# Optimization experiments

Hardware: AMD Instinct MI355X
Metric: run time of the kernel (lower is better)

Reference implementation:

```python
import jax, jax.numpy as jnp
import numpy as np

B, N, E, S, A, P, T = 512, 65536, 131072, 256, 512, 2, 64


def setup_inputs() -> dict:
    key = jax.random.key(0)
    ks = jax.random.split(key, 40)
    f32 = jnp.float32

    def g(i, shape, s=0.05):
        return jax.random.normal(ks[i], shape, f32) * s

    inp = {
        'nodes': jax.random.normal(ks[0], (N, S), f32),
        'edge_features': jax.random.normal(ks[1], (E, S), f32),
        'edge_source': jax.random.randint(ks[2], (E,), 0, N),
        'edge_dest': jax.random.randint(ks[3], (E,), 0, N),
        'node_owner': jax.random.randint(ks[4], (N,), 0, B),
        'running': jnp.ones((B,), bool),
        'ref_types': jax.random.randint(ks[5], (B,), 0, T),
        # decision aggregator (transform + sigmoid gate)
        'dec_t_W': g(6, (A, S)), 'dec_t_b': g(7, (A,)),
        'dec_g_W': g(8, (A, S)), 'dec_g_b': jnp.ones((A,), f32),
        # init aggregator
        'init_t_W': g(9, (A, S)), 'init_t_b': g(10, (A,)),
        'init_g_W': g(11, (A, S)), 'init_g_b': jnp.ones((A,), f32),
        # node type decision head + embedding
        'ntd_W': g(12, (T + 1, A)), 'ntd_b': g(13, (T + 1,)),
        'nte': g(14, (T, S), 1.0),
        # f_init
        'f1_W': g(15, (S, S)), 'f1_b': g(16, (S,)),
        'f2_W': g(17, (S, A)),
        # propagator params, stacked over P steps (message_size = 2S)
        'mn_W': g(18, (P, 2 * S, S)),
        'mf_W': g(19, (P, 2 * S, S)),
        'ml2_W': g(20, (P, 2 * S, 2 * S)), 'ml2_b': g(21, (P, 2 * S)),
        'gru_Wih': g(22, (P, 3 * S, 2 * S)), 'gru_Whh': g(23, (P, 3 * S, S)),
        'gru_bih': jnp.zeros((P, 3 * S), f32),
        'gru_bhh': jnp.concatenate(
            [jnp.ones((P, S), f32), jnp.zeros((P, 2 * S), f32)], axis=-1),
    }
    return inp


def _aggregate(nodes, fmask, tW, tb, gW, gb):
    # Aggregator.forward: sigmoid gate * linear transform, pooled per graph
    # via dense 0/1 owner-mask matmul (dropout=0 -> identity).
    gates = jax.nn.sigmoid(nodes @ gW.T + gb)
    data = nodes @ tW.T + tb
    return fmask @ (data * gates)  # [B, A]


def reference(nodes, edge_features, edge_source, edge_dest, node_owner,
              running, ref_types,
              dec_t_W, dec_t_b, dec_g_W, dec_g_b,
              init_t_W, init_t_b, init_g_W, init_g_b,
              ntd_W, ntd_b, nte, f1_W, f1_b, f2_W,
              mn_W, mf_W, ml2_W, ml2_b, gru_Wih, gru_Whh, gru_bih, gru_bhh):
    f32 = nodes.dtype
    fmask = (node_owner[None, :] == jnp.arange(B)[:, None]).astype(f32)  # [B,N]
    # Propagator._node_update_mask: owner_masks[running].sum(0) > 0
    upd = (fmask * running[:, None].astype(f32)).sum(0) > 0  # [N]

    for p in range(P):
        ef = edge_features @ mf_W[p].T                 # [E, 2S]
        nf = nodes @ mn_W[p].T                         # [N, 2S]
        msgs = nf[edge_source] + nf[edge_dest] + ef
        msgs = jnp.tanh(msgs) @ ml2_W[p].T + ml2_b[p]  # message_layer_2
        inputs = jnp.zeros((N, 2 * S), f32)
        inputs = inputs.at[edge_dest].add(msgs).at[edge_source].add(msgs)
        # torch GRUCell (gate order r, z, n)
        gi = inputs @ gru_Wih[p].T + gru_bih[p]
        gh = nodes @ gru_Whh[p].T + gru_bhh[p]
        ir, iz, inn = jnp.split(gi, 3, axis=-1)
        hr, hz, hn = jnp.split(gh, 3, axis=-1)
        r = jax.nn.sigmoid(ir + hr)
        z = jax.nn.sigmoid(iz + hz)
        n = jnp.tanh(inn + r * hn)
        new_nodes = (1.0 - z) * n + z * nodes
        nodes = jnp.where(upd[:, None], new_nodes, nodes)

    # node-type decision
    agg = _aggregate(nodes, fmask, dec_t_W, dec_t_b, dec_g_W, dec_g_b)
    logits = agg @ ntd_W.T + ntd_b                      # [B, T+1]

    # training path: remap_pad (no pad chars present) -> ref + 1
    sel = ref_types + 1                                  # in [1, T]
    logp = jax.nn.log_softmax(logits, axis=-1)
    per_ex = -logp[jnp.arange(B), sel]
    loss = jnp.where(running, per_ex, 0.0).mean()

    # new node features for running graphs
    emb = nte[sel - 1]                                   # [B, S]
    init_feats = _aggregate(nodes, fmask, init_t_W, init_t_b,
                            init_g_W, init_g_b)
    new_features = emb @ f1_W.T + f1_b + init_feats @ f2_W.T  # [B, S]
    return logits, new_features, loss
```

## Files before the change

kernel.cpp:

```cpp
#include <hip/hip_runtime.h>
#include <hip/hip_bf16.h>
#include <math.h>

#define BG 512
#define NN 65536
#define EE 131072
#define SD 256
#define AD 512
#define PP 2
#define TD 64

typedef __attribute__((ext_vector_type(8))) short sx8;
typedef __attribute__((ext_vector_type(4))) short sx4;
typedef __attribute__((ext_vector_type(4))) float fx4;

__device__ __forceinline__ float bs2f(short s) {
    union { unsigned u; float f; } x; x.u = ((unsigned)(unsigned short)s) << 16; return x.f;
}
__device__ __forceinline__ short f2bs(float f) {
    union { float f; unsigned u; } x; x.f = f;
    unsigned r = x.u + 0x7fffu + ((x.u >> 16) & 1u);
    return (short)(r >> 16);
}
__device__ __forceinline__ float fast_tanh(float x) {
    float xc = fminf(fmaxf(x, -15.f), 15.f);
    float e = __expf(2.f * xc);
    return __fdividef(e - 1.f, e + 1.f);
}
__device__ __forceinline__ float fast_sigm(float x) {
    float xc = fminf(fmaxf(x, -30.f), 30.f);
    float e = __expf(-xc);
    return __fdividef(1.f, 1.f + e);
}
__device__ __forceinline__ bool run_flag(const void* runv, int idx) {
    const unsigned char* r8 = (const unsigned char*)runv;
    const int* r32 = (const int*)runv;
    return (r8[idx] != 0) || (r32[idx] != 0);
}

__device__ __forceinline__ void gload16(const short* g, short* l) {
    __builtin_amdgcn_global_load_lds(
        (const __attribute__((address_space(1))) void*)g,
        (__attribute__((address_space(3))) void*)l, 16, 0, 0);
}

template<int EPI>
__launch_bounds__(256, 4)
__global__ void gemm_bt(const short* __restrict__ Abp, const short* __restrict__ Abp2,
                        const short* __restrict__ Wp,
                        const float* __restrict__ bias, const float* __restrict__ bias2,
                        short* __restrict__ Cout, short* __restrict__ Fout,
                        short* __restrict__ FoutB,
                        const float* __restrict__ biasB, const float* __restrict__ biasB2,
                        const int* __restrict__ degp,
                        int K, int Ksp, int NC, int NT, int nsplit)
{
    __shared__ __align__(16) short sA[2 * 4096];
    __shared__ __align__(16) short sB[2 * 4096];
    const int t = threadIdx.x;
    const int lane = t & 63;
    const int w = t >> 6;

    const int nwg = gridDim.x;
    const int q = nwg >> 3;
    const int wg = (blockIdx.x & 7) * q + (blockIdx.x >> 3);
    const int mt = wg / NT;
    const int nt = wg - mt * NT;
    const int m0 = mt * 128;
    const int n0 = nt * 128;

    const int wm = (w >> 1) * 64;
    const int wn = (w & 1) * 64;
    const int lr = lane & 15;
    const int lg = lane >> 4;

    fx4 acc[4][4];
#pragma unroll
    for (int i = 0; i < 4; i++)
#pragma unroll
        for (int j = 0; j < 4; j++) { fx4 z = {0.f, 0.f, 0.f, 0.f}; acc[i][j] = z; }

    const int r = t >> 2;
    const int cblk = (t & 3) ^ ((r >> 1) & 3);
    const short* gA  = Abp  + (size_t)(m0 + r) * Ksp + cblk * 8;
    const short* gA2 = Abp2 + (size_t)(m0 + r) * (K - Ksp) + cblk * 8;
    const short* gB  = Wp + (size_t)(n0 + r) * K + cblk * 8;
    const size_t rsA  = (size_t)64 * Ksp;
    const size_t rsA2 = (size_t)64 * (K - Ksp);
    const size_t rsB  = (size_t)64 * K;

    auto STAGE = [&](int b, int kk) {
        const short* a0 = (kk < Ksp) ? (gA + kk) : (gA2 + (kk - Ksp));
        const size_t rs = (kk < Ksp) ? rsA : rsA2;
        gload16(a0,            sA + b * 4096 + w * 512);
        gload16(a0 + rs,       sA + b * 4096 + 2048 + w * 512);
        gload16(gB + kk,       sB + b * 4096 + w * 512);
        gload16(gB + kk + rsB, sB + b * 4096 + 2048 + w * 512);
    };

    STAGE(0, 0);

    float dgv[4];
    if (EPI == 3) {
#pragma unroll
        for (int mi = 0; mi < 4; mi++)
            dgv[mi] = (float)degp[m0 + wm + mi * 16 + lr];
    }

    __syncthreads();
    int buf = 0;
    const int xa = (lr >> 1) & 3;
    for (int kk = 0; kk < K; kk += 32) {
        if (kk + 32 < K) STAGE(buf ^ 1, kk + 32);
        const short* cA = sA + buf * 4096;
        const short* cB = sB + buf * 4096;
        sx8 af[4], bfr[4];
#pragma unroll
        for (int mi = 0; mi < 4; mi++)
            af[mi] = *(const sx8*)(cA + (wm + mi * 16 + lr) * 32 + (lg ^ xa) * 8);
#pragma unroll
        for (int ni = 0; ni < 4; ni++)
            bfr[ni] = *(const sx8*)(cB + (wn + ni * 16 + lr) * 32 + (lg ^ xa) * 8);
#pragma unroll
        for (int mi = 0; mi < 4; mi++)
#pragma unroll
            for (int ni = 0; ni < 4; ni++) {
                if (EPI == 4)
                    acc[mi][ni] = __builtin_amdgcn_mfma_f32_16x16x32_bf16(
                        af[mi], bfr[ni], acc[mi][ni], 0, 0, 0);
                else
                    acc[mi][ni] = __builtin_amdgcn_mfma_f32_16x16x32_bf16(
                        bfr[ni], af[mi], acc[mi][ni], 0, 0, 0);
            }
        __syncthreads();
        buf ^= 1;
    }

    if (EPI == 4) {
        const bool useB = (n0 >= nsplit);
        short* fo = useB ? FoutB : Fout;
        const float* tb = useB ? biasB : bias;
        const float* gb = useB ? biasB2 : bias2;
        const int ln0 = useB ? (n0 - nsplit) : n0;
#pragma unroll
        for (int mi = 0; mi < 4; mi++) {
#pragma unroll
            for (int rg = 0; rg < 4; rg++) {
                const int m = m0 + wm + mi * 16 + lg * 4 + rg;
#pragma unroll
                for (int ni = 0; ni < 4; ni += 2) {
                    const int rc = (((ln0 + wn + ni * 16) >> 5) << 4) + lr;
                    float dv = acc[mi][ni][rg] + tb[rc];
                    float gv = fast_sigm(acc[mi][ni + 1][rg] + gb[rc]);
                    fo[(size_t)m * 512 + rc] = f2bs(dv * gv);
                }
            }
        }
    } else {
#pragma unroll
        for (int mi = 0; mi < 4; mi++) {
            const int m = m0 + wm + mi * 16 + lr;
            short* co = Cout + (size_t)m * NC + n0;
#pragma unroll
            for (int ni = 0; ni < 4; ni++) {
                const int nc = wn + ni * 16 + lg * 4;
                sx4 o;
                if (EPI == 1) {
#pragma unroll
                    for (int rg = 0; rg < 4; rg++)
                        o[rg] = f2bs(fast_tanh(acc[mi][ni][rg]));
                } else if (EPI == 3) {
                    fx4 bv = *(const fx4*)(bias + n0 + nc);
                    fx4 cv = *(const fx4*)(bias2 + n0 + nc);
#pragma unroll
                    for (int rg = 0; rg < 4; rg++)
                        o[rg] = f2bs(acc[mi][ni][rg] + dgv[mi] * cv[rg] + bv[rg]);
                } else {
                    fx4 vb = {0.f, 0.f, 0.f, 0.f};
                    if (bias) vb = *(const fx4*)(bias + n0 + nc);
#pragma unroll
                    for (int rg = 0; rg < 4; rg++)
                        o[rg] = f2bs(acc[mi][ni][rg] + vb[rg]);
                }
                *(sx4*)(co + nc) = o;
            }
        }
    }
}

__global__ void k_xadd(const short* __restrict__ nodes, const int* __restrict__ esrc,
                       const int* __restrict__ edst, short* __restrict__ X)
{
    size_t idx = ((size_t)blockIdx.x * 256 + threadIdx.x) * 8;
    const int e = (int)(idx >> 8);
    const int j = (int)(idx & 255);
    const int s = esrc[e], d = edst[e];
    sx8 a = *(const sx8*)(nodes + (size_t)s * 256 + j);
    sx8 b = *(const sx8*)(nodes + (size_t)d * 256 + j);
    sx8 o;
#pragma unroll
    for (int u = 0; u < 8; u++) o[u] = f2bs(bs2f(a[u]) + bs2f(b[u]));
    *(sx8*)(X + idx) = o;
}

__global__ void k_castw(const float* __restrict__ in, short* __restrict__ out)
{
    size_t i = ((size_t)blockIdx.x * 256 + threadIdx.x) * 4;
    fx4 v = *(const fx4*)(in + i);
    sx4 o;
#pragma unroll
    for (int u = 0; u < 4; u++) o[u] = f2bs(v[u]);
    *(sx4*)(out + i) = o;
}

__global__ void k_cast_T(const float* __restrict__ in, short* __restrict__ out)
{
    size_t i = ((size_t)blockIdx.x * 256 + threadIdx.x) * 4;
    const int k = (int)(i >> 9);
    const int k2 = (int)(i & 511);
    sx4 o;
#pragma unroll
    for (int u = 0; u < 4; u++) o[u] = f2bs(in[(size_t)(k2 + u) * 512 + k]);
    *(sx4*)(out + i) = o;
}

__global__ void k_vecfuse(const float* __restrict__ Wih, const float* __restrict__ ml2b,
                          float* __restrict__ c1)
{
    const int i = blockIdx.x * 256 + threadIdx.x;
    if (i >= 768) return;
    const float* wr = Wih + (size_t)i * 512;
    float acc = 0.f;
    for (int k = 0; k < 512; k++) acc += wr[k] * ml2b[k];
    c1[i] = acc;
}

__global__ void k_cast_comb(const float* __restrict__ mn, const float* __restrict__ mf,
                            short* __restrict__ out)
{
    size_t i = ((size_t)blockIdx.x * 256 + threadIdx.x) * 4;
    const int n = (int)(i >> 9);
    const int k = (int)(i & 511);
    const float* W = (k < 256) ? (mn + (size_t)n * 256 + k)
                               : (mf + (size_t)n * 256 + (k - 256));
    fx4 v = *(const fx4*)W;
    sx4 o;
#pragma unroll
    for (int u = 0; u < 4; u++) o[u] = f2bs(v[u]);
    *(sx4*)(out + i) = o;
}

__global__ void k_cast_pair(const float* __restrict__ tW, const float* __restrict__ gW,
                            short* __restrict__ out)
{
    size_t i = ((size_t)blockIdx.x * 256 + threadIdx.x) * 4;
    const int r2 = (int)(i >> 8);
    const int c = (int)(i & 255);
    const int src = ((r2 >> 5) << 4) | (r2 & 15);
    const float* W = ((r2 >> 4) & 1) ? gW : tW;
    fx4 v = *(const fx4*)(W + (size_t)src * 256 + c);
    sx4 o;
#pragma unroll
    for (int u = 0; u < 4; u++) o[u] = f2bs(v[u]);
    *(sx4*)(out + i) = o;
}

__global__ void k_count2(const int* __restrict__ a, const int* __restrict__ b,
                         int* __restrict__ deg, int n)
{
    int i = blockIdx.x * 256 + threadIdx.x;
    if (i < n) { atomicAdd(&deg[a[i]], 1); atomicAdd(&deg[b[i]], 1); }
}
__global__ void k_count1(const int* __restrict__ a, int* __restrict__ deg, int n)
{
    int i = blockIdx.x * 256 + threadIdx.x;
    if (i < n) atomicAdd(&deg[a[i]], 1);
}
__global__ void k_scan(const int* __restrict__ deg, int* __restrict__ offs, int n)
{
    __shared__ int part[256];
    const int t = threadIdx.x;
    const int chunk = n >> 8;
    const int base = t * chunk;
    int s = 0;
    for (int i = 0; i < chunk; i++) s += deg[base + i];
    part[t] = s;
    __syncthreads();
    for (int off = 1; off < 256; off <<= 1) {
        int v = (t >= off) ? part[t - off] : 0;
        __syncthreads();
        part[t] += v;
        __syncthreads();
    }
    int run = (t > 0) ? part[t - 1] : 0;
    for (int i = 0; i < chunk; i++) {
        offs[base + i] = run;
        run += deg[base + i];
    }
    if (t == 255) offs[n] = part[255];
}
__global__ void k_fill2(const int* __restrict__ a, const int* __restrict__ b,
                        const int* __restrict__ offs, int* __restrict__ cur,
                        int* __restrict__ elist, int n)
{
    int i = blockIdx.x * 256 + threadIdx.x;
    if (i < n) {
        int p = atomicAdd(&cur[a[i]], 1); elist[offs[a[i]] + p] = i;
        int q = atomicAdd(&cur[b[i]], 1); elist[offs[b[i]] + q] = i;
    }
}
__global__ void k_fill1(const int* __restrict__ own, const int* __restrict__ offs,
                        int* __restrict__ cur, int* __restrict__ nlist, int n)
{
    int i = blockIdx.x * 256 + threadIdx.x;
    if (i < n) {
        int p = atomicAdd(&cur[own[i]], 1); nlist[offs[own[i]] + p] = i;
    }
}

__global__ void k_edge_gather(const short* __restrict__ msgs, const int* __restrict__ offs,
                              const int* __restrict__ elist, short* __restrict__ inp)
{
    const int node = blockIdx.x * 4 + (threadIdx.x >> 6);
    const int c = (threadIdx.x & 63) * 8;
    const int s0 = offs[node], s1 = offs[node + 1];
    float acc[8] = {0.f, 0.f, 0.f, 0.f, 0.f, 0.f, 0.f, 0.f};
    for (int s = s0; s < s1; s++) {
        const int e = elist[s];
        sx8 v = *(const sx8*)(msgs + (size_t)e * 512 + c);
#pragma unroll
        for (int u = 0; u < 8; u++) acc[u] += bs2f(v[u]);
    }
    sx8 o;
#pragma unroll
    for (int u = 0; u < 8; u++) o[u] = f2bs(acc[u]);
    *(sx8*)(inp + (size_t)node * 512 + c) = o;
}

__global__ void k_owner_reduce(const short* __restrict__ gp, const int* __restrict__ offsB,
                               const int* __restrict__ nlist, float* __restrict__ agg)
{
    const int b = blockIdx.x, t = threadIdx.x;
    const int s0 = offsB[b], s1 = offsB[b + 1];
    float a0 = 0.f, a1 = 0.f;
    for (int s = s0; s < s1; s++) {
        const int n = nlist[s];
        const short* pp = gp + (size_t)n * 512 + t * 2;
        a0 += bs2f(pp[0]); a1 += bs2f(pp[1]);
    }
    agg[(size_t)b * 512 + t * 2] = a0;
    agg[(size_t)b * 512 + t * 2 + 1] = a1;
}

__global__ void k_gru(const short* __restrict__ gi, const short* __restrict__ gh,
                      short* __restrict__ nodes,
                      const int* __restrict__ owner, const void* __restrict__ runv)
{
    const int n = blockIdx.x * 4 + (threadIdx.x >> 6);
    const int t = threadIdx.x & 63;
    const bool run = run_flag(runv, owner[n]);
    const size_t gb = (size_t)n * 768 + t * 4;
    sx4 vir = *(const sx4*)(gi + gb);
    sx4 viz = *(const sx4*)(gi + gb + 256);
    sx4 vin = *(const sx4*)(gi + gb + 512);
    sx4 whr = *(const sx4*)(gh + gb);
    sx4 whz = *(const sx4*)(gh + gb + 256);
    sx4 whn = *(const sx4*)(gh + gb + 512);
    const size_t nbase = (size_t)n * 256 + t * 4;
    sx4 old4 = *(const sx4*)(nodes + nbase);
    sx4 outb;
#pragma unroll
    for (int u = 0; u < 4; u++) {
        float old = bs2f(old4[u]);
        float rr = fast_sigm(bs2f(vir[u]) + bs2f(whr[u]));
        float zz = fast_sigm(bs2f(viz[u]) + bs2f(whz[u]));
        float nn = fast_tanh(bs2f(vin[u]) + rr * bs2f(whn[u]));
        float nv = (1.f - zz) * nn + zz * old;
        outb[u] = run ? f2bs(nv) : old4[u];
    }
    *(sx4*)(nodes + nbase) = outb;
}

__global__ void k_logits(const float* __restrict__ agg, const float* __restrict__ Wt,
                         const float* __restrict__ bt, float* __restrict__ logitsF,
                         float* __restrict__ outL)
{
    __shared__ float row[512];
    const int b = blockIdx.x, t = threadIdx.x;
    for (int k = t; k < 512; k += 128) row[k] = agg[(size_t)b * 512 + k];
    __syncthreads();
    if (t < TD + 1) {
        float acc = bt[t];
        const float* wr = Wt + (size_t)t * 512;
        for (int k = 0; k < 512; k++) acc += row[k] * wr[k];
        logitsF[b * (TD + 1) + t] = acc;
        outL[b * (TD + 1) + t] = acc;
    }
}

__global__ void k_loss(const float* __restrict__ logitsF, const int* __restrict__ reft,
                       const void* __restrict__ runv, float* __restrict__ outLoss)
{
    __shared__ float red[512];
    const int b = threadIdx.x;
    const float* lr = logitsF + b * (TD + 1);
    float mx = lr[0];
    for (int k = 1; k < TD + 1; k++) mx = fmaxf(mx, lr[k]);
    float se = 0.f;
    for (int k = 0; k < TD + 1; k++) se += expf(lr[k] - mx);
    const int sel = reft[b] + 1;
    float pe = logf(se) + mx - lr[sel];
    red[b] = run_flag(runv, b) ? pe : 0.f;
    __syncthreads();
    for (int s = 256; s > 0; s >>= 1) {
        if (b < s) red[b] += red[b + s];
        __syncthreads();
    }
    if (b == 0) outLoss[0] = red[0] / (float)BG;
}

__global__ void k_newfeat(const float* __restrict__ aggi, const float* __restrict__ nte,
                          const int* __restrict__ reft, const float* __restrict__ f1W,
                          const float* __restrict__ f1b, const float* __restrict__ f2W,
                          float* __restrict__ outNF)
{
    __shared__ float emb[256];
    __shared__ float ag[512];
    const int b = blockIdx.x, t = threadIdx.x;
    const int rt = reft[b];
    emb[t] = nte[(size_t)rt * 256 + t];
    ag[t] = aggi[(size_t)b * 512 + t];
    ag[t + 256] = aggi[(size_t)b * 512 + 256 + t];
    __syncthreads();
    float acc = f1b[t];
    const float* w1 = f1W + (size_t)t * 256;
    for (int k = 0; k < 256; k++) acc += emb[k] * w1[k];
    const float* w2 = f2W + (size_t)t * 512;
    for (int a = 0; a < 512; a++) acc += ag[a] * w2[a];
    outNF[(size_t)b * 256 + t] = acc;
}

extern "C" void kernel_launch(void* const* d_in, const int* in_sizes, int n_in,
                              void* d_out, int out_size, void* d_ws, size_t ws_size,
                              hipStream_t stream)
{
    (void)in_sizes; (void)n_in; (void)out_size;
    const float* in_nodes = (const float*)d_in[0];
    const float* in_ef    = (const float*)d_in[1];
    const int*   e_src    = (const int*)d_in[2];
    const int*   e_dst    = (const int*)d_in[3];
    const int*   owner    = (const int*)d_in[4];
    const void*  running  = d_in[5];
    const int*   reft     = (const int*)d_in[6];
    const float* dec_tW = (const float*)d_in[7];
    const float* dec_tb = (const float*)d_in[8];
    const float* dec_gW = (const float*)d_in[9];
    const float* dec_gb = (const float*)d_in[10];
    const float* init_tW = (const float*)d_in[11];
    const float* init_tb = (const float*)d_in[12];
    const float* init_gW = (const float*)d_in[13];
    const float* init_gb = (const float*)d_in[14];
    const float* ntdW = (const float*)d_in[15];
    const float* ntdb = (const float*)d_in[16];
    const float* nte  = (const float*)d_in[17];
    const float* f1W  = (const float*)d_in[18];
    const float* f1b  = (const float*)d_in[19];
    const float* f2W  = (const float*)d_in[20];
    const float* mnW  = (const float*)d_in[21];
    const float* mfW  = (const float*)d_in[22];
    const float* ml2W = (const float*)d_in[23];
    const float* ml2b = (const float*)d_in[24];
    const float* Wih  = (const float*)d_in[25];
    const float* Whh  = (const float*)d_in[26];
    const float* bih  = (const float*)d_in[27];
    const float* bhh  = (const float*)d_in[28];

    float* outL    = (float*)d_out;
    float* outNF   = outL + BG * (TD + 1);
    float* outLoss = outNF + BG * SD;

    size_t off = 0;
    auto take = [&](size_t bytes) -> void* {
        void* p = (char*)d_ws + off;
        off += (bytes + 255) & ~(size_t)255;
        return p;
    };
    short* nodes_bf  = (short*)take((size_t)NN * SD * 2);
    short* ef_bf     = (short*)take((size_t)EE * SD * 2);
    short* bufC      = (short*)take((size_t)EE * SD * 2);
    short* bufD      = (short*)take((size_t)EE * 512 * 2);
    short* bufM      = (short*)take((size_t)EE * 512 * 2);
    short* bufI      = (short*)take((size_t)NN * 512 * 2);
    float* aggD      = (float*)take((size_t)BG * AD * 4);
    float* aggI      = (float*)take((size_t)BG * AD * 4);
    float* logitsF   = (float*)take((size_t)BG * (TD + 1) * 4);
    short* WcombB = (short*)take((size_t)PP * 512 * 512 * 2);
    short* ml2Tb  = (short*)take((size_t)512 * 512 * 2);
    short* WfB    = (short*)take((size_t)PP * 768 * 512 * 2);
    float* c1f    = (float*)take((size_t)PP * 768 * 4);
    short* WihB  = (short*)take((size_t)PP * 768 * 512 * 2);
    short* WhhB  = (short*)take((size_t)PP * 768 * 256 * 2);
    short* W4agg = (short*)take((size_t)2048 * 256 * 2);
    int* deg_e = (int*)take((size_t)NN * 4);
    int* offs_e = (int*)take((size_t)(NN + 1) * 4);
    int* cur_e = (int*)take((size_t)NN * 4);
    int* elist = (int*)take((size_t)2 * EE * 4);
    int* degB = (int*)take((size_t)BG * 4);
    int* offsB = (int*)take((size_t)(BG + 1) * 4);
    int* curB = (int*)take((size_t)BG * 4);
    int* nlist = (int*)take((size_t)NN * 4);
    if (off > ws_size) return;

    short* gi = bufD;
    short* gh = bufM;
    short* gpD = bufM;
    short* gpI = bufD;

    k_castw<<<NN * SD / 1024, 256, 0, stream>>>(in_nodes, nodes_bf);
    k_castw<<<EE * SD / 1024, 256, 0, stream>>>(in_ef, ef_bf);
    for (int p = 0; p < PP; p++)
        k_cast_comb<<<512 * 512 / 1024, 256, 0, stream>>>(
            mnW + (size_t)p * 512 * 256, mfW + (size_t)p * 512 * 256,
            WcombB + (size_t)p * 512 * 512);
    k_castw<<<PP * 768 * 512 / 1024, 256, 0, stream>>>(Wih, WihB);
    k_castw<<<PP * 768 * 256 / 1024, 256, 0, stream>>>(Whh, WhhB);
    k_cast_pair<<<1024 * 256 / 1024, 256, 0, stream>>>(dec_tW, dec_gW, W4agg);
    k_cast_pair<<<1024 * 256 / 1024, 256, 0, stream>>>(init_tW, init_gW,
                                                       W4agg + 1024 * 256);
    for (int p = 0; p < PP; p++) {
        k_cast_T<<<512 * 512 / 1024, 256, 0, stream>>>(
            ml2W + (size_t)p * 512 * 512, ml2Tb);
        gemm_bt<0><<<768 / 128 * 4, 256, 0, stream>>>(
            WihB + (size_t)p * 768 * 512, WihB + (size_t)p * 768 * 512, ml2Tb,
            nullptr, nullptr, WfB + (size_t)p * 768 * 512,
            nullptr, nullptr, nullptr, nullptr, nullptr,
            512, 512, 512, 4, 0);
        k_vecfuse<<<3, 256, 0, stream>>>(Wih + (size_t)p * 768 * 512,
                                         ml2b + (size_t)p * 512, c1f + p * 768);
    }

    hipMemsetAsync(deg_e, 0, (size_t)NN * 4, stream);
    hipMemsetAsync(cur_e, 0, (size_t)NN * 4, stream);
    hipMemsetAsync(degB, 0, (size_t)BG * 4, stream);
    hipMemsetAsync(curB, 0, (size_t)BG * 4, stream);
    k_count2<<<(EE + 255) / 256, 256, 0, stream>>>(e_src, e_dst, deg_e, EE);
    k_scan<<<1, 256, 0, stream>>>(deg_e, offs_e, NN);
    k_fill2<<<(EE + 255) / 256, 256, 0, stream>>>(e_src, e_dst, offs_e, cur_e, elist, EE);
    k_count1<<<(NN + 255) / 256, 256, 0, stream>>>(owner, degB, NN);
    k_scan<<<1, 256, 0, stream>>>(degB, offsB, BG);
    k_fill1<<<(NN + 255) / 256, 256, 0, stream>>>(owner, offsB, curB, nlist, NN);

    for (int p = 0; p < PP; p++) {
        k_xadd<<<EE / 8, 256, 0, stream>>>(nodes_bf, e_src, e_dst, bufC);
        gemm_bt<1><<<EE / 128 * 4, 256, 0, stream>>>(
            bufC, ef_bf, WcombB + (size_t)p * 512 * 512, nullptr, nullptr,
            bufD, nullptr, nullptr, nullptr, nullptr, nullptr,
            512, 256, 512, 4, 0);
        k_edge_gather<<<NN / 4, 256, 0, stream>>>(bufD, offs_e, elist, bufI);
        gemm_bt<3><<<NN / 128 * 6, 256, 0, stream>>>(
            bufI, bufI, WfB + (size_t)p * 768 * 512,
            bih + (size_t)p * 768, c1f + p * 768,
            gi, nullptr, nullptr, nullptr, nullptr, deg_e,
            512, 512, 768, 6, 0);
        gemm_bt<0><<<NN / 128 * 6, 256, 0, stream>>>(
            nodes_bf, nodes_bf, WhhB + (size_t)p * 768 * 256, bhh + (size_t)p * 768,
            nullptr, gh, nullptr, nullptr, nullptr, nullptr, nullptr,
            256, 256, 768, 6, 0);
        k_gru<<<NN / 4, 256, 0, stream>>>(gi, gh, nodes_bf, owner, running);
    }

    gemm_bt<4><<<NN / 128 * 16, 256, 0, stream>>>(
        nodes_bf, nodes_bf, W4agg, dec_tb, dec_gb,
        nullptr, gpD, gpI, init_tb, init_gb, nullptr,
        256, 256, 2048, 16, 1024);
    k_owner_reduce<<<BG, 256, 0, stream>>>(gpD, offsB, nlist, aggD);
    k_owner_reduce<<<BG, 256, 0, stream>>>(gpI, offsB, nlist, aggI);

    k_logits<<<BG, 128, 0, stream>>>(aggD, ntdW, ntdb, logitsF, outL);
    k_loss<<<1, 512, 0, stream>>>(logitsF, reft, running, outLoss);
    k_newfeat<<<BG, 256, 0, stream>>>(aggI, nte, reft, f1W, f1b, f2W, outNF);
}
```

Baseline: 1.659 ms.

## Merge GRU input and hidden GEMMs into one concatenated-K GEMM

Builds a combined 1024x768 weight that stacks the folded input weights (K=512) and the hidden weights Whh (K=256) along K. Its r and z rows are summed and the hidden-n rows are kept separate. Biases are precombined to match. One GEMM over [aggregated inputs | nodes] replaces the two separate gi/gh GEMMs, and the GRU kernel now reads 4 gate slices instead of 6. This removes one launch and some output traffic, but adds zero-padded FLOPs in the n-gate blocks. It also relies on the gemm kernel handling the two-source A operand split at K=512.

```diff
diff --git a/kernel.cpp b/kernel.cpp
--- a/kernel.cpp
+++ b/kernel.cpp
@@ -233,6 +233,33 @@
     float acc = 0.f;
     for (int k = 0; k < 512; k++) acc += wr[k] * ml2b[k];
     c1[i] = acc;
+}
+
+__global__ void k_fill_gru(const short* __restrict__ Whh, short* __restrict__ out)
+{
+    size_t idx = ((size_t)blockIdx.x * 256 + threadIdx.x) * 4;
+    const int o = (int)(idx / 768);
+    const int k = (int)(idx % 768);
+    if (o < 768 && k < 512) return;
+    sx4 v = {0, 0, 0, 0};
+    if (k >= 512) {
+        if (o < 512)       v = *(const sx4*)(Whh + (size_t)o * 256 + (k - 512));
+        else if (o >= 768) v = *(const sx4*)(Whh + (size_t)(o - 256) * 256 + (k - 512));
+    }
+    *(sx4*)(out + idx) = v;
+}
+
+__global__ void k_grubias(const float* __restrict__ bih, const float* __restrict__ bhh,
+                          const float* __restrict__ c1,
+                          float* __restrict__ bg, float* __restrict__ cg)
+{
+    const int o = blockIdx.x * 256 + threadIdx.x;
+    if (o >= 1024) return;
+    float b, c;
+    if (o < 512)      { b = bih[o] + bhh[o]; c = c1[o]; }
+    else if (o < 768) { b = bih[o];          c = c1[o]; }
+    else              { b = bhh[o - 256];    c = 0.f;   }
+    bg[o] = b; cg[o] = c;
 }
 
 __global__ void k_cast_comb(const float* __restrict__ mn, const float* __restrict__ mf,
@@ -352,29 +379,26 @@
     agg[(size_t)b * 512 + t * 2 + 1] = a1;
 }
 
-__global__ void k_gru(const short* __restrict__ gi, const short* __restrict__ gh,
-                      short* __restrict__ nodes,
+__global__ void k_gru(const short* __restrict__ G, short* __restrict__ nodes,
                       const int* __restrict__ owner, const void* __restrict__ runv)
 {
     const int n = blockIdx.x * 4 + (threadIdx.x >> 6);
     const int t = threadIdx.x & 63;
     const bool run = run_flag(runv, owner[n]);
-    const size_t gb = (size_t)n * 768 + t * 4;
-    sx4 vir = *(const sx4*)(gi + gb);
-    sx4 viz = *(const sx4*)(gi + gb + 256);
-    sx4 vin = *(const sx4*)(gi + gb + 512);
-    sx4 whr = *(const sx4*)(gh + gb);
-    sx4 whz = *(const sx4*)(gh + gb + 256);
-    sx4 whn = *(const sx4*)(gh + gb + 512);
+    const size_t gb = (size_t)n * 1024 + t * 4;
+    sx4 grr = *(const sx4*)(G + gb);
+    sx4 grz = *(const sx4*)(G + gb + 256);
+    sx4 gin = *(const sx4*)(G + gb + 512);
+    sx4 ghn = *(const sx4*)(G + gb + 768);
     const size_t nbase = (size_t)n * 256 + t * 4;
     sx4 old4 = *(const sx4*)(nodes + nbase);
     sx4 outb;
 #pragma unroll
     for (int u = 0; u < 4; u++) {
         float old = bs2f(old4[u]);
-        float rr = fast_sigm(bs2f(vir[u]) + bs2f(whr[u]));
-        float zz = fast_sigm(bs2f(viz[u]) + bs2f(whz[u]));
-        float nn = fast_tanh(bs2f(vin[u]) + rr * bs2f(whn[u]));
+        float rr = fast_sigm(bs2f(grr[u]));
+        float zz = fast_sigm(bs2f(grz[u]));
+        float nn = fast_tanh(bs2f(gin[u]) + rr * bs2f(ghn[u]));
         float nv = (1.f - zz) * nn + zz * old;
         outb[u] = run ? f2bs(nv) : old4[u];
     }
@@ -496,8 +520,10 @@
     float* logitsF   = (float*)take((size_t)BG * (TD + 1) * 4);
     short* WcombB = (short*)take((size_t)PP * 512 * 512 * 2);
     short* ml2Tb  = (short*)take((size_t)512 * 512 * 2);
-    short* WfB    = (short*)take((size_t)PP * 768 * 512 * 2);
+    short* WgruB  = (short*)take((size_t)PP * 1024 * 768 * 2);
     float* c1f    = (float*)take((size_t)PP * 768 * 4);
+    float* bgru   = (float*)take((size_t)PP * 1024 * 4);
+    float* cgru   = (float*)take((size_t)PP * 1024 * 4);
     short* WihB  = (short*)take((size_t)PP * 768 * 512 * 2);
     short* WhhB  = (short*)take((size_t)PP * 768 * 256 * 2);
     short* W4agg = (short*)take((size_t)2048 * 256 * 2);
@@ -511,8 +537,7 @@
     int* nlist = (int*)take((size_t)NN * 4);
     if (off > ws_size) return;
 
-    short* gi = bufD;
-    short* gh = bufM;
+    short* G   = bufD;
     short* gpD = bufM;
     short* gpI = bufD;
 
@@ -532,11 +557,15 @@
             ml2W + (size_t)p * 512 * 512, ml2Tb);
         gemm_bt<0><<<768 / 128 * 4, 256, 0, stream>>>(
             WihB + (size_t)p * 768 * 512, WihB + (size_t)p * 768 * 512, ml2Tb,
-            nullptr, nullptr, WfB + (size_t)p * 768 * 512,
+            nullptr, nullptr, WgruB + (size_t)p * 1024 * 768,
             nullptr, nullptr, nullptr, nullptr, nullptr,
-            512, 512, 512, 4, 0);
+            512, 512, 768, 4, 0);
         k_vecfuse<<<3, 256, 0, stream>>>(Wih + (size_t)p * 768 * 512,
                                          ml2b + (size_t)p * 512, c1f + p * 768);
+        k_fill_gru<<<1024 * 768 / 4 / 256, 256, 0, stream>>>(
+            WhhB + (size_t)p * 768 * 256, WgruB + (size_t)p * 1024 * 768);
+        k_grubias<<<4, 256, 0, stream>>>(bih + (size_t)p * 768, bhh + (size_t)p * 768,
+                                         c1f + p * 768, bgru + p * 1024, cgru + p * 1024);
     }
 
     hipMemsetAsync(deg_e, 0, (size_t)NN * 4, stream);
@@ -557,16 +586,12 @@
             bufD, nullptr, nullptr, nullptr, nullptr, nullptr,
             512, 256, 512, 4, 0);
         k_edge_gather<<<NN / 4, 256, 0, stream>>>(bufD, offs_e, elist, bufI);
-        gemm_bt<3><<<NN / 128 * 6, 256, 0, stream>>>(
-            bufI, bufI, WfB + (size_t)p * 768 * 512,
-            bih + (size_t)p * 768, c1f + p * 768,
-            gi, nullptr, nullptr, nullptr, nullptr, deg_e,
-            512, 512, 768, 6, 0);
-        gemm_bt<0><<<NN / 128 * 6, 256, 0, stream>>>(
-            nodes_bf, nodes_bf, WhhB + (size_t)p * 768 * 256, bhh + (size_t)p * 768,
-            nullptr, gh, nullptr, nullptr, nullptr, nullptr, nullptr,
-            256, 256, 768, 6, 0);
-        k_gru<<<NN / 4, 256, 0, stream>>>(gi, gh, nodes_bf, owner, running);
+        gemm_bt<3><<<NN / 128 * 8, 256, 0, stream>>>(
+            bufI, nodes_bf, WgruB + (size_t)p * 1024 * 768,
+            bgru + p * 1024, cgru + p * 1024,
+            G, nullptr, nullptr, nullptr, nullptr, deg_e,
+            768, 512, 1024, 8, 0);
+        k_gru<<<NN / 4, 256, 0, stream>>>(G, nodes_bf, owner, running);
     }
 
     gemm_bt<4><<<NN / 128 * 16, 256, 0, stream>>>(
```

Result: faster. 1.626 ms (-2.0%).
